# Optimization experiments

Measured on AMD Instinct MI355X. Metric: run time of the kernel, lower is better.

The kernel has to match this reference:

```python
import jax, jax.numpy as jnp
from jax import lax
import numpy as np

N_INPUTS = 2048
UNITS = 2048
L = 8
FANIN = 4096
TOTAL = N_INPUTS + L * UNITS  # 18432, size of flattened outputs vector


def setup_inputs() -> dict:
    key = jax.random.key(0)
    k1, k2, k3, k4 = jax.random.split(key, 4)
    x = jax.random.normal(k1, (N_INPUTS,), dtype=jnp.float32)
    node_inds = jax.random.randint(k2, (L, FANIN), 0, TOTAL, dtype=jnp.int32)
    # 0.02 scale keeps tanh out of deep saturation (matches small evolved weights)
    Ws = jax.random.normal(k3, (L, FANIN, UNITS), dtype=jnp.float32) * 0.02
    bs = jax.random.normal(k4, (L, UNITS), dtype=jnp.float32) * 0.02
    return {"x": x, "node_inds": node_inds, "Ws": Ws, "bs": bs}


def reference(x, node_inds, Ws, bs):
    # Flattened shared state vector, zero-initialized like the tf.Variable.
    outputs = jnp.zeros((TOTAL,), dtype=x.dtype)
    start = 0  # static python offset: out_update_inds are contiguous ranges
    for i in range(L):
        # scatter_nd_update of x into contiguous slice == dynamic_update_slice
        outputs = lax.dynamic_update_slice(outputs, x, (start,))
        start += x.shape[0]
        # gather node-specific indices then tiny Dense + tanh
        gathered = jnp.take(outputs, node_inds[i])          # [FANIN]
        x = jnp.tanh(gathered @ Ws[i] + bs[i])              # [UNITS]
    return x
```

## Files before the change

kernel.cpp:

```cpp
#include <hip/hip_runtime.h>
#include <cmath>

#define N_INPUTS 2048
#define UNITS    2048
#define L_LAYERS 8
#define FANIN    4096
#define TOTAL    18432

#define NTHREADS 256
#define RK       16
#define KC       (FANIN / RK)
#define JTILE    1024
#define P_BLOCKS (2 * KC)

__device__ __forceinline__ float col_reduce(const float* __restrict__ P, int col)
{
    int lane = threadIdx.x & 63;
    float s = 0.f;
    #pragma unroll
    for (int m = 0; m < KC / 64; ++m)
        s += P[(size_t)(lane + m * 64) * UNITS + col];
    #pragma unroll
    for (int off = 32; off; off >>= 1)
        s += __shfl_down(s, off, 64);
    return __shfl(s, 0, 64);
}

__global__ __launch_bounds__(NTHREADS) void layer_kernel(
    int layer,
    const float* __restrict__ x,
    const int*   __restrict__ node_inds,
    const float* __restrict__ Ws,
    const float* __restrict__ bs,
    float*       __restrict__ outputs,
    const float* __restrict__ Pprev,
    float*       __restrict__ Pcur)
{
    const int b    = blockIdx.x;
    const int t    = threadIdx.x;
    const int wv   = t >> 6;
    const int lane = t & 63;
    const int jhalf = b & 1;
    const int kc    = b >> 1;

    __shared__ float gsh[RK];

    {
        int col = b * 4 + wv;
        if (layer == 0) {
            if (lane == 0) outputs[col] = x[col];
        } else {
            float s = col_reduce(Pprev, col);
            float y = tanhf(s + bs[(layer - 1) * UNITS + col]);
            if (lane == 0) outputs[(size_t)layer * UNITS + col] = y;
        }
    }

    #pragma unroll
    for (int j = 0; j < 4; ++j) {
        int q   = wv * 4 + j;
        int idx = node_inds[layer * FANIN + kc * RK + q];
        float g;
        if (layer == 0) {
            g = (idx < N_INPUTS) ? x[idx] : 0.f;
        } else if (idx < layer * UNITS) {
            g = outputs[idx];
        } else if (idx < (layer + 1) * UNITS) {
            int col = idx - layer * UNITS;
            float s = col_reduce(Pprev, col);
            g = tanhf(s + bs[(layer - 1) * UNITS + col]);
        } else {
            g = 0.f;
        }
        if (lane == 0) gsh[q] = g;
    }
    __syncthreads();

    const int jbase = jhalf * JTILE + t * 4;
    const float4* W4 = (const float4*)(
        Ws + ((size_t)layer * FANIN + (size_t)kc * RK) * UNITS + jbase);

    float4 a; a.x = 0.f; a.y = 0.f; a.z = 0.f; a.w = 0.f;
    #pragma unroll
    for (int k = 0; k < RK; ++k) {
        float  g = gsh[k];
        float4 w = W4[(size_t)k * (UNITS / 4)];
        a.x += g * w.x; a.y += g * w.y; a.z += g * w.z; a.w += g * w.w;
    }
    *(float4*)(Pcur + (size_t)kc * UNITS + jbase) = a;
}

__global__ __launch_bounds__(NTHREADS) void tail_kernel(
    const float* __restrict__ Pprev,
    const float* __restrict__ bs,
    float*       __restrict__ out)
{
    int wv   = threadIdx.x >> 6;
    int lane = threadIdx.x & 63;
    int col  = blockIdx.x * 4 + wv;
    float s = col_reduce(Pprev, col);
    float y = tanhf(s + bs[(L_LAYERS - 1) * UNITS + col]);
    if (lane == 0) out[col] = y;
}

extern "C" void kernel_launch(void* const* d_in, const int* in_sizes, int n_in,
                              void* d_out, int out_size, void* d_ws, size_t ws_size,
                              hipStream_t stream) {
    const float* x         = (const float*)d_in[0];
    const int*   node_inds = (const int*)  d_in[1];
    const float* Ws        = (const float*)d_in[2];
    const float* bs        = (const float*)d_in[3];
    float*       out       = (float*)d_out;
    float*       ws        = (float*)d_ws;

    float* outputs = ws;
    float* P0      = ws + TOTAL;
    float* P1      = P0 + (size_t)KC * UNITS;

    float* pbuf[2] = { P0, P1 };

    for (int i = 0; i < L_LAYERS; ++i) {
        layer_kernel<<<P_BLOCKS, NTHREADS, 0, stream>>>(
            i, x, node_inds, Ws, bs, outputs,
            pbuf[(i + 1) & 1],
            pbuf[i & 1]);
    }
    tail_kernel<<<UNITS / 4, NTHREADS, 0, stream>>>(
        pbuf[(L_LAYERS - 1) & 1], bs, out);
}
```

Baseline: 416.9 us.

## Fuse all layers into one persistent kernel with grid barriers and weight prefetch

Replaces the eight per-layer launches plus tail launch with a single persistent kernel of 512 blocks that loops over layers and synchronises with an atomic-counter grid barrier. Each thread also prefetches the next layer's weight tile into registers before the barrier, so the weight stream overlaps barrier waiting. This is meant to remove kernel launch gaps and let the memory-bound weight reads overlap. The catch is that correctness depends on all 512 blocks being co-resident; otherwise the barrier deadlocks. Spin-wait atomics add their own latency.

```diff
diff --git a/kernel.cpp b/kernel.cpp
--- a/kernel.cpp
+++ b/kernel.cpp
@@ -11,7 +11,7 @@
 #define RK       16
 #define KC       (FANIN / RK)
 #define JTILE    1024
-#define P_BLOCKS (2 * KC)
+#define NBLOCKS  (2 * KC)
 
 __device__ __forceinline__ float col_reduce(const float* __restrict__ P, int col)
 {
@@ -26,15 +26,35 @@
     return __shfl(s, 0, 64);
 }
 
-__global__ __launch_bounds__(NTHREADS) void layer_kernel(
-    int layer,
+__device__ __forceinline__ void grid_barrier(int* cnt)
+{
+    __syncthreads();
+    if (threadIdx.x == 0) {
+        __threadfence();
+        __hip_atomic_fetch_add(cnt, 1, __ATOMIC_RELEASE, __HIP_MEMORY_SCOPE_AGENT);
+        while (__hip_atomic_load(cnt, __ATOMIC_ACQUIRE, __HIP_MEMORY_SCOPE_AGENT) < NBLOCKS)
+            __builtin_amdgcn_s_sleep(8);
+        __threadfence();
+    }
+    __syncthreads();
+    asm volatile("" ::: "memory");
+}
+
+__global__ void init_kernel(int* __restrict__ cnt)
+{
+    if (threadIdx.x < L_LAYERS) cnt[threadIdx.x] = 0;
+}
+
+__global__ __launch_bounds__(NTHREADS, 2) void net_kernel(
     const float* __restrict__ x,
     const int*   __restrict__ node_inds,
     const float* __restrict__ Ws,
     const float* __restrict__ bs,
+    float*       __restrict__ out,
     float*       __restrict__ outputs,
-    const float* __restrict__ Pprev,
-    float*       __restrict__ Pcur)
+    float*       __restrict__ P0,
+    float*       __restrict__ P1,
+    int*         __restrict__ cnt)
 {
     const int b    = blockIdx.x;
     const int t    = threadIdx.x;
@@ -42,65 +62,76 @@
     const int lane = t & 63;
     const int jhalf = b & 1;
     const int kc    = b >> 1;
+    const int jbase = jhalf * JTILE + t * 4;
+    const int col   = b * 4 + wv;
 
     __shared__ float gsh[RK];
 
+    float4 w[RK];
     {
-        int col = b * 4 + wv;
-        if (layer == 0) {
+        const float4* W4 = (const float4*)(Ws + (size_t)kc * RK * UNITS + jbase);
+        #pragma unroll
+        for (int k = 0; k < RK; ++k)
+            w[k] = W4[(size_t)k * (UNITS / 4)];
+    }
+
+    for (int i = 0; i < L_LAYERS; ++i) {
+        const float* Pprev = (i & 1) ? P0 : P1;
+        float*       Pcur  = (i & 1) ? P1 : P0;
+
+        if (i == 0) {
             if (lane == 0) outputs[col] = x[col];
         } else {
             float s = col_reduce(Pprev, col);
-            float y = tanhf(s + bs[(layer - 1) * UNITS + col]);
-            if (lane == 0) outputs[(size_t)layer * UNITS + col] = y;
+            float y = tanhf(s + bs[(i - 1) * UNITS + col]);
+            if (lane == 0) outputs[(size_t)i * UNITS + col] = y;
         }
+
+        #pragma unroll
+        for (int j = 0; j < 4; ++j) {
+            int q   = wv * 4 + j;
+            int idx = node_inds[i * FANIN + kc * RK + q];
+            float g;
+            if (i == 0) {
+                g = (idx < N_INPUTS) ? x[idx] : 0.f;
+            } else if (idx < i * UNITS) {
+                g = outputs[idx];
+            } else if (idx < (i + 1) * UNITS) {
+                int c = idx - i * UNITS;
+                float s = col_reduce(Pprev, c);
+                g = tanhf(s + bs[(i - 1) * UNITS + c]);
+            } else {
+                g = 0.f;
+            }
+            if (lane == 0) gsh[q] = g;
+        }
+        __syncthreads();
+
+        float4 a; a.x = 0.f; a.y = 0.f; a.z = 0.f; a.w = 0.f;
+        #pragma unroll
+        for (int k = 0; k < RK; ++k) {
+            float g = gsh[k];
+            a.x += g * w[k].x; a.y += g * w[k].y;
+            a.z += g * w[k].z; a.w += g * w[k].w;
+        }
+        *(float4*)(Pcur + (size_t)kc * UNITS + jbase) = a;
+
+        if (i + 1 < L_LAYERS) {
+            const float4* W4 = (const float4*)(
+                Ws + ((size_t)(i + 1) * FANIN + (size_t)kc * RK) * UNITS + jbase);
+            #pragma unroll
+            for (int k = 0; k < RK; ++k)
+                w[k] = W4[(size_t)k * (UNITS / 4)];
+        }
+
+        grid_barrier(&cnt[i]);
     }
 
-    #pragma unroll
-    for (int j = 0; j < 4; ++j) {
-        int q   = wv * 4 + j;
-        int idx = node_inds[layer * FANIN + kc * RK + q];
-        float g;
-        if (layer == 0) {
-            g = (idx < N_INPUTS) ? x[idx] : 0.f;
-        } else if (idx < layer * UNITS) {
-            g = outputs[idx];
-        } else if (idx < (layer + 1) * UNITS) {
-            int col = idx - layer * UNITS;
-            float s = col_reduce(Pprev, col);
-            g = tanhf(s + bs[(layer - 1) * UNITS + col]);
-        } else {
-            g = 0.f;
-        }
-        if (lane == 0) gsh[q] = g;
+    {
+        float s = col_reduce(P1, col);
+        float y = tanhf(s + bs[(L_LAYERS - 1) * UNITS + col]);
+        if (lane == 0) out[col] = y;
     }
-    __syncthreads();
-
-    const int jbase = jhalf * JTILE + t * 4;
-    const float4* W4 = (const float4*)(
-        Ws + ((size_t)layer * FANIN + (size_t)kc * RK) * UNITS + jbase);
-
-    float4 a; a.x = 0.f; a.y = 0.f; a.z = 0.f; a.w = 0.f;
-    #pragma unroll
-    for (int k = 0; k < RK; ++k) {
-        float  g = gsh[k];
-        float4 w = W4[(size_t)k * (UNITS / 4)];
-        a.x += g * w.x; a.y += g * w.y; a.z += g * w.z; a.w += g * w.w;
-    }
-    *(float4*)(Pcur + (size_t)kc * UNITS + jbase) = a;
-}
-
-__global__ __launch_bounds__(NTHREADS) void tail_kernel(
-    const float* __restrict__ Pprev,
-    const float* __restrict__ bs,
-    float*       __restrict__ out)
-{
-    int wv   = threadIdx.x >> 6;
-    int lane = threadIdx.x & 63;
-    int col  = blockIdx.x * 4 + wv;
-    float s = col_reduce(Pprev, col);
-    float y = tanhf(s + bs[(L_LAYERS - 1) * UNITS + col]);
-    if (lane == 0) out[col] = y;
 }
 
 extern "C" void kernel_launch(void* const* d_in, const int* in_sizes, int n_in,
@@ -114,17 +145,11 @@
     float*       ws        = (float*)d_ws;
 
     float* outputs = ws;
-    float* P0      = ws + TOTAL;
+    float* P0      = outputs + TOTAL;
     float* P1      = P0 + (size_t)KC * UNITS;
+    int*   cnt     = (int*)(P1 + (size_t)KC * UNITS);
 
-    float* pbuf[2] = { P0, P1 };
-
-    for (int i = 0; i < L_LAYERS; ++i) {
-        layer_kernel<<<P_BLOCKS, NTHREADS, 0, stream>>>(
-            i, x, node_inds, Ws, bs, outputs,
-            pbuf[(i + 1) & 1],
-            pbuf[i & 1]);
-    }
-    tail_kernel<<<UNITS / 4, NTHREADS, 0, stream>>>(
-        pbuf[(L_LAYERS - 1) & 1], bs, out);
+    init_kernel<<<1, 64, 0, stream>>>(cnt);
+    net_kernel<<<NBLOCKS, NTHREADS, 0, stream>>>(
+        x, node_inds, Ws, bs, out, outputs, P0, P1, cnt);
 }
```

Measured after the change: 1.201 ms. +188.2%, slower.
